# Performance work log

Hardware: AMD Instinct MI355X
Metric: run time of the kernel (lower is better)

Reference implementation:

```python
import jax, jax.numpy as jnp
import numpy as np

IGNORE = 250
EPS = 1e-8


def setup_inputs() -> dict:
    key = jax.random.key(0)
    k1, k2 = jax.random.split(key)
    B, P, H, W, C = 8, 200, 256, 256, 20
    prototype_distances = jax.random.normal(k1, (B, P, H, W), dtype=jnp.float32)
    # ProtoPNet-style identity: prototype p belongs to class p // (P//C)
    proto_classes = jnp.arange(P) // (P // C)
    prototype_class_identity = jax.nn.one_hot(proto_classes, C, dtype=jnp.float32)  # [P, C]
    target_labels = jax.random.randint(k2, (B, H, W), 0, C, dtype=jnp.int32)
    return {
        "prototype_distances": prototype_distances,
        "prototype_class_identity": prototype_class_identity,
        "target_labels": target_labels,
    }


def reference(prototype_distances, prototype_class_identity, target_labels):
    B, P, H, W = prototype_distances.shape
    C = prototype_class_identity.shape[1]

    act = jax.nn.softmax(-prototype_distances, axis=1)            # [B,P,H,W]
    # Faithful to torch: prototype_activations.view(num_prototypes, -1).t()
    acts_flat = act.reshape(P, -1).T                               # [N, P], N = B*H*W
    labels = target_labels.reshape(-1)                             # [N]
    valid = labels != IGNORE

    k = jnp.sum(prototype_class_identity == 1, axis=0)            # [C] protos per class
    has_proto = k > 0
    k_safe = jnp.maximum(k, 1).astype(jnp.float32)
    # target_dist[c, p] = 1/k_c where identity[p,c]==1 else 0
    T = jnp.where(prototype_class_identity.T == 1, 1.0 / k_safe[:, None], 0.0)  # [C,P]
    # sum_p T log T = -log(k_c) when k_c > 0
    ent = jnp.where(has_proto, -jnp.log(k_safe), 0.0)             # [C]

    log_act = jnp.log(acts_flat + EPS)                            # [N,P]
    labels_safe = jnp.clip(labels, 0, C - 1)
    T_pix = T[labels_safe]                                        # [N,P]
    # KL(target || act) per pixel, reduction='sum'
    per_pix = ent[labels_safe] - jnp.sum(T_pix * log_act, axis=-1)  # [N]

    counted = valid & has_proto[labels_safe]
    count = jnp.sum(counted).astype(jnp.float32)
    total = jnp.sum(jnp.where(counted, per_pix, 0.0))
    return jnp.where(count > 0, total / jnp.maximum(count, 1.0), 0.0)
```

## Files before the change

### kernel.cpp

```cpp
#include <hip/hip_runtime.h>

#define B_  8
#define P_  200
#define HW_ 65536
#define CPP 80

typedef __attribute__((ext_vector_type(4))) float f32x4;
typedef __attribute__((ext_vector_type(4))) int   i32x4;


__global__ __launch_bounds__(256) void kl_main(const float* __restrict__ dist,
                                               const int* __restrict__ labels,
                                               double* __restrict__ acc_sum,
                                               unsigned int* __restrict__ acc_cnt) {
    int idx = blockIdx.x * 256 + threadIdx.x;
    int b   = idx >> 14;
    int hwq = idx & 16383;

    int lab[8][4];
#pragma unroll
    for (int nh = 0; nh < 8; ++nh) {
        i32x4 l = ((const i32x4*)(labels + nh * HW_))[hwq];
        lab[nh][0] = l.x; lab[nh][1] = l.y; lab[nh][2] = l.z; lab[nh][3] = l.w;
    }

    const f32x4* dp = (const f32x4*)(dist + (size_t)b * P_ * HW_) + hwq;
    const int qb = b * P_;

    float s[4]  = {0.f, 0.f, 0.f, 0.f};
    float sx[4] = {0.f, 0.f, 0.f, 0.f};
    int   c[4]  = {0, 0, 0, 0};

    for (int g = 0; g < P_ / 8; ++g) {
#pragma unroll
        for (int r = 0; r < 8; ++r) {
            int p0 = g * 8 + r;
            f32x4 v = __builtin_nontemporal_load(dp + (size_t)p0 * (HW_ / 4));
            int cls = (unsigned)(qb + p0) / (unsigned)CPP;
            float e0 = __expf(-v.x), e1 = __expf(-v.y),
                  e2 = __expf(-v.z), e3 = __expf(-v.w);
            s[0] += e0; s[1] += e1; s[2] += e2; s[3] += e3;
            if (lab[r][0] == cls) { sx[0] -= v.x; ++c[0]; }
            if (lab[r][1] == cls) { sx[1] -= v.y; ++c[1]; }
            if (lab[r][2] == cls) { sx[2] -= v.z; ++c[2]; }
            if (lab[r][3] == cls) { sx[3] -= v.w; ++c[3]; }
        }
    }

    float part = (sx[0] - (float)c[0] * __logf(s[0]))
               + (sx[1] - (float)c[1] * __logf(s[1]))
               + (sx[2] - (float)c[2] * __logf(s[2]))
               + (sx[3] - (float)c[3] * __logf(s[3]));
    int cnt = c[0] + c[1] + c[2] + c[3];

#pragma unroll
    for (int off = 32; off > 0; off >>= 1) {
        part += __shfl_down(part, off);
        cnt  += __shfl_down(cnt, off);
    }
    __shared__ float sp[4];
    __shared__ int   sc[4];
    int wid = threadIdx.x >> 6;
    if ((threadIdx.x & 63) == 0) { sp[wid] = part; sc[wid] = cnt; }
    __syncthreads();
    if (threadIdx.x == 0) {
        double t = (double)sp[0] + (double)sp[1] + (double)sp[2] + (double)sp[3];
        unsigned int ct = (unsigned int)(sc[0] + sc[1] + sc[2] + sc[3]);
        atomicAdd(acc_sum, t);
        atomicAdd(acc_cnt, ct);
    }
}

__global__ void kl_final(const double* __restrict__ acc_sum,
                         const unsigned int* __restrict__ acc_cnt,
                         float* __restrict__ out) {
    double s = *acc_sum;
    unsigned int c = *acc_cnt;
    out[0] = (c > 0u) ? (float)(-2.302585092994046 - s / (double)c) : 0.0f;
}

extern "C" void kernel_launch(void* const* d_in, const int* in_sizes, int n_in,
                              void* d_out, int out_size, void* d_ws, size_t ws_size,
                              hipStream_t stream) {
    const float* dist  = (const float*)d_in[0];
    const int* labels  = (const int*)d_in[2];
    float* out = (float*)d_out;

    double*       acc_sum = (double*)d_ws;
    unsigned int* acc_cnt = (unsigned int*)((char*)d_ws + 8);

    (void)hipMemsetAsync(d_ws, 0, 16, stream);

    const int total_threads = B_ * (HW_ / 4);
    kl_main<<<total_threads / 256, 256, 0, stream>>>(dist, labels, acc_sum, acc_cnt);
    kl_final<<<1, 1, 0, stream>>>(acc_sum, acc_cnt, out);
}
```

Baseline: 76.82 us.

## Split prototype reduction across two half-waves per pixel column

Doubles the thread count so that two half-waves share each pixel column, with each half handling alternating groups of 8 prototypes. Partial exp sums are combined with a cross-lane xor shuffle before the log. This is meant to raise memory-level parallelism and occupancy for the bandwidth-bound pass over 400MB. In exchange it adds a shuffle, makes the two halves do unequal work on the tail group, and launches more blocks, which means more atomics.

```diff
diff --git a/kernel.cpp b/kernel.cpp
--- a/kernel.cpp
+++ b/kernel.cpp
@@ -14,8 +14,10 @@
                                                double* __restrict__ acc_sum,
                                                unsigned int* __restrict__ acc_cnt) {
     int idx = blockIdx.x * 256 + threadIdx.x;
-    int b   = idx >> 14;
-    int hwq = idx & 16383;
+    int h   = (idx >> 5) & 1;
+    int col = ((idx >> 6) << 5) | (idx & 31);
+    int b   = col >> 14;
+    int hwq = col & 16383;
 
     int lab[8][4];
 #pragma unroll
@@ -31,15 +33,29 @@
     float sx[4] = {0.f, 0.f, 0.f, 0.f};
     int   c[4]  = {0, 0, 0, 0};
 
-    for (int g = 0; g < P_ / 8; ++g) {
+    for (int t = 0; t < 12; ++t) {
+        int gbase = 16 * t + 8 * h;
 #pragma unroll
         for (int r = 0; r < 8; ++r) {
-            int p0 = g * 8 + r;
+            int p0 = gbase + r;
             f32x4 v = __builtin_nontemporal_load(dp + (size_t)p0 * (HW_ / 4));
             int cls = (unsigned)(qb + p0) / (unsigned)CPP;
-            float e0 = __expf(-v.x), e1 = __expf(-v.y),
-                  e2 = __expf(-v.z), e3 = __expf(-v.w);
-            s[0] += e0; s[1] += e1; s[2] += e2; s[3] += e3;
+            s[0] += __expf(-v.x); s[1] += __expf(-v.y);
+            s[2] += __expf(-v.z); s[3] += __expf(-v.w);
+            if (lab[r][0] == cls) { sx[0] -= v.x; ++c[0]; }
+            if (lab[r][1] == cls) { sx[1] -= v.y; ++c[1]; }
+            if (lab[r][2] == cls) { sx[2] -= v.z; ++c[2]; }
+            if (lab[r][3] == cls) { sx[3] -= v.w; ++c[3]; }
+        }
+    }
+    if (h == 0) {
+#pragma unroll
+        for (int r = 0; r < 8; ++r) {
+            int p0 = 192 + r;
+            f32x4 v = __builtin_nontemporal_load(dp + (size_t)p0 * (HW_ / 4));
+            int cls = (unsigned)(qb + p0) / (unsigned)CPP;
+            s[0] += __expf(-v.x); s[1] += __expf(-v.y);
+            s[2] += __expf(-v.z); s[3] += __expf(-v.w);
             if (lab[r][0] == cls) { sx[0] -= v.x; ++c[0]; }
             if (lab[r][1] == cls) { sx[1] -= v.y; ++c[1]; }
             if (lab[r][2] == cls) { sx[2] -= v.z; ++c[2]; }
@@ -47,10 +63,12 @@
         }
     }
 
-    float part = (sx[0] - (float)c[0] * __logf(s[0]))
-               + (sx[1] - (float)c[1] * __logf(s[1]))
-               + (sx[2] - (float)c[2] * __logf(s[2]))
-               + (sx[3] - (float)c[3] * __logf(s[3]));
+    float part = 0.f;
+#pragma unroll
+    for (int k = 0; k < 4; ++k) {
+        float st = s[k] + __shfl_xor(s[k], 32);
+        part += sx[k] - (float)c[k] * __logf(st);
+    }
     int cnt = c[0] + c[1] + c[2] + c[3];
 
 #pragma unroll
@@ -91,7 +109,7 @@
 
     (void)hipMemsetAsync(d_ws, 0, 16, stream);
 
-    const int total_threads = B_ * (HW_ / 4);
+    const int total_threads = 2 * B_ * (HW_ / 4);
     kl_main<<<total_threads / 256, 256, 0, stream>>>(dist, labels, acc_sum, acc_cnt);
     kl_final<<<1, 1, 0, stream>>>(acc_sum, acc_cnt, out);
 }
```

Result: slower. 87.23 us (+13.5%).

## Split prototype loop across two thread halves per pixel group

Applied to the files above, without the earlier changes.

Each block now covers 128 pixel quads, and two threads share each quad: one handles prototypes 0-103 and the other 104-199. Partial exp-sums, target sums and counts from the first half go through shared memory to the second half, which combines them before the log and the reductions. This doubles the number of threads and in-flight loads to improve memory-level parallelism for a bandwidth-bound stream. The cost is extra shared memory, an added barrier and a launch-bounds occupancy hint.

```diff
diff --git a/kernel.cpp b/kernel.cpp
--- a/kernel.cpp
+++ b/kernel.cpp
@@ -9,11 +9,14 @@
 typedef __attribute__((ext_vector_type(4))) int   i32x4;
 
 
-__global__ __launch_bounds__(256) void kl_main(const float* __restrict__ dist,
-                                               const int* __restrict__ labels,
-                                               double* __restrict__ acc_sum,
-                                               unsigned int* __restrict__ acc_cnt) {
-    int idx = blockIdx.x * 256 + threadIdx.x;
+__global__ __launch_bounds__(256, 4) void kl_main(const float* __restrict__ dist,
+                                                  const int* __restrict__ labels,
+                                                  double* __restrict__ acc_sum,
+                                                  unsigned int* __restrict__ acc_cnt) {
+    int tid = threadIdx.x;
+    int ph  = tid >> 7;
+    int lq  = tid & 127;
+    int idx = blockIdx.x * 128 + lq;
     int b   = idx >> 14;
     int hwq = idx & 16383;
 
@@ -26,20 +29,21 @@
 
     const f32x4* dp = (const f32x4*)(dist + (size_t)b * P_ * HW_) + hwq;
     const int qb = b * P_;
+    const int p_begin = ph ? 104 : 0;
+    const int n_grp   = ph ? 12 : 13;
 
     float s[4]  = {0.f, 0.f, 0.f, 0.f};
     float sx[4] = {0.f, 0.f, 0.f, 0.f};
     int   c[4]  = {0, 0, 0, 0};
 
-    for (int g = 0; g < P_ / 8; ++g) {
+    for (int g = 0; g < n_grp; ++g) {
 #pragma unroll
         for (int r = 0; r < 8; ++r) {
-            int p0 = g * 8 + r;
+            int p0 = p_begin + g * 8 + r;
             f32x4 v = __builtin_nontemporal_load(dp + (size_t)p0 * (HW_ / 4));
             int cls = (unsigned)(qb + p0) / (unsigned)CPP;
-            float e0 = __expf(-v.x), e1 = __expf(-v.y),
-                  e2 = __expf(-v.z), e3 = __expf(-v.w);
-            s[0] += e0; s[1] += e1; s[2] += e2; s[3] += e3;
+            s[0] += __expf(-v.x); s[1] += __expf(-v.y);
+            s[2] += __expf(-v.z); s[3] += __expf(-v.w);
             if (lab[r][0] == cls) { sx[0] -= v.x; ++c[0]; }
             if (lab[r][1] == cls) { sx[1] -= v.y; ++c[1]; }
             if (lab[r][2] == cls) { sx[2] -= v.z; ++c[2]; }
@@ -47,27 +51,39 @@
         }
     }
 
-    float part = (sx[0] - (float)c[0] * __logf(s[0]))
-               + (sx[1] - (float)c[1] * __logf(s[1]))
-               + (sx[2] - (float)c[2] * __logf(s[2]))
-               + (sx[3] - (float)c[3] * __logf(s[3]));
-    int cnt = c[0] + c[1] + c[2] + c[3];
+    __shared__ float s_l[128][5];
+    __shared__ float sx_l[128][5];
+    __shared__ int   c_l[128][5];
+    if (ph == 0) {
+#pragma unroll
+        for (int k = 0; k < 4; ++k) { s_l[lq][k] = s[k]; sx_l[lq][k] = sx[k]; c_l[lq][k] = c[k]; }
+    }
+    __syncthreads();
 
+    __shared__ float pacc[2];
+    __shared__ int   cacc[2];
+    if (ph == 1) {
+        float part = 0.f;
+        int cnt = 0;
 #pragma unroll
-    for (int off = 32; off > 0; off >>= 1) {
-        part += __shfl_down(part, off);
-        cnt  += __shfl_down(cnt, off);
+        for (int k = 0; k < 4; ++k) {
+            float st = s[k] + s_l[lq][k];
+            int   ct = c[k] + c_l[lq][k];
+            part += (sx[k] + sx_l[lq][k]) - (float)ct * __logf(st);
+            cnt  += ct;
+        }
+#pragma unroll
+        for (int off = 32; off > 0; off >>= 1) {
+            part += __shfl_down(part, off);
+            cnt  += __shfl_down(cnt, off);
+        }
+        int w = (tid >> 6) - 2;
+        if ((tid & 63) == 0) { pacc[w] = part; cacc[w] = cnt; }
     }
-    __shared__ float sp[4];
-    __shared__ int   sc[4];
-    int wid = threadIdx.x >> 6;
-    if ((threadIdx.x & 63) == 0) { sp[wid] = part; sc[wid] = cnt; }
     __syncthreads();
-    if (threadIdx.x == 0) {
-        double t = (double)sp[0] + (double)sp[1] + (double)sp[2] + (double)sp[3];
-        unsigned int ct = (unsigned int)(sc[0] + sc[1] + sc[2] + sc[3]);
-        atomicAdd(acc_sum, t);
-        atomicAdd(acc_cnt, ct);
+    if (tid == 0) {
+        atomicAdd(acc_sum, (double)pacc[0] + (double)pacc[1]);
+        atomicAdd(acc_cnt, (unsigned int)(cacc[0] + cacc[1]));
     }
 }
 
@@ -91,7 +107,7 @@
 
     (void)hipMemsetAsync(d_ws, 0, 16, stream);
 
-    const int total_threads = B_ * (HW_ / 4);
-    kl_main<<<total_threads / 256, 256, 0, stream>>>(dist, labels, acc_sum, acc_cnt);
+    const int n_blocks = (B_ * (HW_ / 4)) / 128;
+    kl_main<<<n_blocks, 256, 0, stream>>>(dist, labels, acc_sum, acc_cnt);
     kl_final<<<1, 1, 0, stream>>>(acc_sum, acc_cnt, out);
 }
```

Result: slower. 80.55 us (+4.8%).
